# Kernel tuning notes

Measured on AMD Instinct MI355X. Metric: run time of the kernel, lower is better.

## Reference

```python
import jax, jax.numpy as jnp
import numpy as np
from jax import lax

EPS = 1e-5  # torch LayerNorm / BatchNorm1d default eps
HEADS, DH, DEPTH, C = 4, 128, 2, 512


def setup_inputs() -> dict:
    key = jax.random.key(0)
    ks = iter(jax.random.split(key, 48))
    def rn(shape, scale=1.0):
        return jax.random.normal(next(ks), shape, jnp.float32) * scale
    d, L = 1024, DEPTH
    inp = {}
    inp['x'] = rn((16, 10, 256, d))                      # (b, ncrops, T, d)
    # Temporal embedding: Conv1d(d -> 512, k=3, pad=1) + ReLU
    inp['W_emb'] = rn((C, d, 3), (d * 3) ** -0.5)
    inp['b_emb'] = jnp.zeros((C,), jnp.float32)
    # Transformer (depth=2), params stacked along layer axis
    inp['ln1_g'] = jnp.ones((L, C), jnp.float32); inp['ln1_b'] = jnp.zeros((L, C), jnp.float32)
    inp['W_qkv'] = rn((L, C, 4 * HEADS * DH), C ** -0.5)  # to_qkv (no bias), inner_dim*4 = 2048
    inp['W_o']  = rn((L, 2 * HEADS * DH, C), (2 * HEADS * DH) ** -0.5)
    inp['b_o']  = jnp.zeros((L, C), jnp.float32)
    inp['ln2_g'] = jnp.ones((L, C), jnp.float32); inp['ln2_b'] = jnp.zeros((L, C), jnp.float32)
    inp['W_f1'] = rn((L, C, C), C ** -0.5); inp['b_f1'] = jnp.zeros((L, C), jnp.float32)
    inp['W_f2'] = rn((L, C, C), C ** -0.5); inp['b_f2'] = jnp.zeros((L, C), jnp.float32)
    # NormalHead: conv1 512->32 (k=1), bn1, conv2 32->16 (k=1), bn2, conv3 16->1 (k=1)
    inp['c1_W'] = rn((32, C), C ** -0.5); inp['c1_b'] = jnp.zeros((32,), jnp.float32)
    inp['bn1_g'] = jnp.ones((32,), jnp.float32); inp['bn1_b'] = jnp.zeros((32,), jnp.float32)
    inp['bn1_m'] = rn((32,), 0.1)
    inp['bn1_v'] = jax.random.uniform(next(ks), (32,), jnp.float32, 0.5, 1.5)
    inp['c2_W'] = rn((16, 32), 32 ** -0.5); inp['c2_b'] = jnp.zeros((16,), jnp.float32)
    inp['bn2_g'] = jnp.ones((16,), jnp.float32); inp['bn2_b'] = jnp.zeros((16,), jnp.float32)
    inp['bn2_m'] = rn((16,), 0.1)
    inp['bn2_v'] = jax.random.uniform(next(ks), (16,), jnp.float32, 0.5, 1.5)
    inp['c3_W'] = rn((1, 16), 0.25); inp['c3_b'] = jnp.zeros((1,), jnp.float32)
    return inp


def _ln(z, g, b):
    m = z.mean(-1, keepdims=True)
    v = ((z - m) ** 2).mean(-1, keepdims=True)
    return (z - m) / jnp.sqrt(v + EPS) * g + b


def _bn_eval(z, g, b, m, v):  # z: (B, C, T), eval-mode BatchNorm1d
    return (z - m[None, :, None]) / jnp.sqrt(v[None, :, None] + EPS) * g[None, :, None] + b[None, :, None]


def _k1conv(z, W, b):  # pointwise Conv1d: z (B, Ci, T), W (Co, Ci)
    return jnp.einsum('bct,oc->bot', z, W) + b[None, :, None]


def reference(x, W_emb, b_emb, ln1_g, ln1_b, W_qkv, W_o, b_o, ln2_g, ln2_b,
              W_f1, b_f1, W_f2, b_f2, c1_W, c1_b, bn1_g, bn1_b, bn1_m, bn1_v,
              c2_W, c2_b, bn2_g, bn2_b, bn2_m, bn2_v, c3_W, c3_b):
    b, n, T, d = x.shape
    h = x.reshape(b * n, T, d)
    # Temporal embedding: Conv1d(k=3, pad=1) + ReLU
    h = lax.conv_general_dilated(h.transpose(0, 2, 1), W_emb, (1,), 'SAME',
                                 dimension_numbers=('NCH', 'OIH', 'NCH'))
    h = jax.nn.relu(h + b_emb[None, :, None]).transpose(0, 2, 1)  # (BN, T, 512)

    # fixed positional-decay attention map attn2 (T, T), batch-independent
    idx = jnp.arange(T, dtype=jnp.float32)
    tg = jnp.abs(idx[None, :] - idx[:, None])
    a2 = jnp.exp(-tg / jnp.exp(1.0))
    a2 = a2 / a2.sum(-1)  # NOTE: broadcast over last axis, exactly as in the torch code

    scale = DH ** -0.5
    for l in range(DEPTH):
        z = _ln(h, ln1_g[l], ln1_b[l])
        qkvt = z @ W_qkv[l]                                   # (BN, T, 2048)
        q, k, v, t = jnp.split(qkvt, 4, axis=-1)
        def to_heads(u):
            return u.reshape(u.shape[0], T, HEADS, DH).transpose(0, 2, 1, 3)
        q, k, v, t = map(to_heads, (q, k, v, t))              # (BN, H, T, DH)
        attn1 = jax.nn.softmax(jnp.einsum('bhid,bhjd->bhij', q, k) * scale, axis=-1)
        o1 = jnp.einsum('bhij,bhjd->bhid', attn1, v)
        o2 = jnp.einsum('ij,bhjd->bhid', a2, t)
        o = jnp.concatenate([o1, o2], axis=-1)                # (BN, H, T, 2*DH)
        o = o.transpose(0, 2, 1, 3).reshape(h.shape[0], T, HEADS * 2 * DH)
        h = o @ W_o[l] + b_o[l] + h                           # attn residual
        z = _ln(h, ln2_g[l], ln2_b[l])
        h = (jax.nn.gelu(z @ W_f1[l] + b_f1[l], approximate=False) @ W_f2[l] + b_f2[l]) + h

    # NormalHead on (BN, C, T)
    f = h.transpose(0, 2, 1)
    x1 = _k1conv(f, c1_W, c1_b)                               # (BN, 32, T)
    x2 = _k1conv(jax.nn.relu(_bn_eval(x1, bn1_g, bn1_b, bn1_m, bn1_v)), c2_W, c2_b)  # (BN, 16, T)
    scores = jax.nn.sigmoid(_k1conv(jax.nn.relu(_bn_eval(x2, bn2_g, bn2_b, bn2_m, bn2_v)), c3_W, c3_b))
    normal_scores = scores.reshape(b, n, T).mean(1)           # mean over ncrops -> (b, T)

    def maha(feats, anchor, var):  # Mahalanobis distance vs BN running stats (no eps, as in source)
        dist = jnp.sqrt(jnp.sum((feats - anchor[None, :, None]) ** 2 / var[None, :, None], axis=1))
        return dist.reshape(b, n, T).mean(1)

    distance_sum = maha(x1, bn1_m, bn1_v) + maha(x2, bn2_m, bn2_v)
    return distance_sum * normal_scores                       # (b, T)
```

## Files before the change

kernel.cpp:

```cpp
#include <hip/hip_runtime.h>
#include <math.h>

#define T_    256
#define D_    1024
#define C_    512
#define H_    4
#define DH_   128
#define BNB   160
#define LEPS  1e-5f
#define INV_E 0.36787944117144233f
#define SCALE_ 0.08838834764831845f
#define LDT   40
#define XROW  264192

typedef unsigned short ushort;
typedef unsigned int   uint;
typedef __attribute__((ext_vector_type(8))) short short8;
typedef __attribute__((ext_vector_type(4))) float f32x4;

__device__ __forceinline__ ushort f2b(float f) {
    uint u = __float_as_uint(f);
    u += 0x7fffu + ((u >> 16) & 1u);
    return (ushort)(u >> 16);
}
__device__ __forceinline__ float b2f(ushort u) {
    return __uint_as_float(((uint)u) << 16);
}
__device__ __forceinline__ uint pk(float a, float b) {
    return (uint)f2b(a) | ((uint)f2b(b) << 16);
}
__device__ __forceinline__ void gl2lds(const void* g, void* l) {
    __builtin_amdgcn_global_load_lds(
        (const __attribute__((address_space(1))) void*)g,
        (__attribute__((address_space(3))) void*)l, 16, 0, 0);
}

__global__ void zero_k(float* __restrict__ p, int n) {
    int i = blockIdx.x * 256 + threadIdx.x;
    if (i < n) p[i] = 0.0f;
}

__global__ void xcvt_k(const float* __restrict__ src, ushort* __restrict__ dst, int n4) {
    int i = blockIdx.x * 256 + threadIdx.x;
    if (i < n4) {
        float4 f = ((const float4*)src)[i];
        uint2 v;
        v.x = pk(f.x, f.y);
        v.y = pk(f.z, f.w);
        int e   = i * 4;
        int bn  = e >> 18;
        int rem = e & 262143;
        ((uint2*)(dst + (size_t)bn * XROW + 1024 + rem))[0] = v;
    }
}

__global__ void xpad_k(ushort* __restrict__ dst, int nbn) {
    int i = blockIdx.x * 256 + threadIdx.x;
    if (i >= nbn * 1024) return;
    int bn = i >> 10, j = i & 1023;
    int r = j >> 9, c = j & 511;
    uint* base = (uint*)(dst + (size_t)bn * XROW);
    base[(r ? (XROW - 1024) / 2 : 0) + c] = 0u;
}

__global__ __launch_bounds__(256)
void tconv_k(const float* __restrict__ src, ushort* __restrict__ dst,
             int K, int N) {
    __shared__ float tile[32][33];
    int kb = blockIdx.x * 32, nb = blockIdx.y * 32;
    int tx = threadIdx.x & 31, ty = threadIdx.x >> 5;
#pragma unroll
    for (int i = 0; i < 32; i += 8)
        tile[ty + i][tx] = src[(size_t)(kb + ty + i) * N + nb + tx];
    __syncthreads();
#pragma unroll
    for (int i = 0; i < 32; i += 8)
        dst[(size_t)(nb + ty + i) * K + kb + tx] = f2b(tile[tx][ty + i]);
}

__global__ void bcvt_k(const float* __restrict__ src, ushort* __restrict__ dst, int n) {
    int i = blockIdx.x * 256 + threadIdx.x;
    if (i < n) dst[i] = f2b(src[i]);
}

__global__ void wemb_k(const float* __restrict__ W, ushort* __restrict__ Wt) {
    int idx = blockIdx.x * 256 + threadIdx.x;
    if (idx >= C_ * 3072) return;
    int c = idx / 3072, k = idx % 3072;
    int dt = k >> 10, ci = k & 1023;
    Wt[idx] = f2b(W[(size_t)c * 3072 + ci * 3 + dt]);
}

__global__ void a2_colsum_k(float* __restrict__ s) {
    int j = threadIdx.x;
    float acc = 0.0f;
    for (int k = 0; k < T_; k++) acc += expf(-fabsf((float)(j - k)) * INV_E);
    s[j] = acc;
}

__global__ void a2fill_k(const float* __restrict__ s, ushort* __restrict__ A2) {
    int i = blockIdx.x, j = threadIdx.x;
    A2[i * 256 + j] = f2b(expf(-fabsf((float)(i - j)) * INV_E) / s[j]);
}

__global__ __launch_bounds__(256)
void ln_k(const ushort* __restrict__ X, const float* __restrict__ g,
          const float* __restrict__ b, ushort* __restrict__ Z) {
    int row  = blockIdx.x * 4 + (threadIdx.x >> 6);
    int lane = threadIdx.x & 63;
    const ushort* xr = X + (size_t)row * C_ + lane * 8;
    uint4 raw = *(const uint4*)xr;
    float f[8];
    f[0] = __uint_as_float(raw.x << 16); f[1] = __uint_as_float(raw.x & 0xffff0000u);
    f[2] = __uint_as_float(raw.y << 16); f[3] = __uint_as_float(raw.y & 0xffff0000u);
    f[4] = __uint_as_float(raw.z << 16); f[5] = __uint_as_float(raw.z & 0xffff0000u);
    f[6] = __uint_as_float(raw.w << 16); f[7] = __uint_as_float(raw.w & 0xffff0000u);
    float s = 0.0f, s2 = 0.0f;
#pragma unroll
    for (int u = 0; u < 8; u++) { s += f[u]; s2 += f[u] * f[u]; }
#pragma unroll
    for (int m = 1; m < 64; m <<= 1) {
        s  += __shfl_xor(s, m);
        s2 += __shfl_xor(s2, m);
    }
    float mean = s * (1.0f / C_);
    float var  = s2 * (1.0f / C_) - mean * mean;
    float rinv = rsqrtf(var + LEPS);
    const float* gp = g + lane * 8;
    const float* bp = b + lane * 8;
    float4 g0 = *(const float4*)gp, g1 = *(const float4*)(gp + 4);
    float4 b0 = *(const float4*)bp, b1 = *(const float4*)(bp + 4);
    uint4 outv;
    outv.x = pk((f[0]-mean)*rinv*g0.x+b0.x, (f[1]-mean)*rinv*g0.y+b0.y);
    outv.y = pk((f[2]-mean)*rinv*g0.z+b0.z, (f[3]-mean)*rinv*g0.w+b0.w);
    outv.z = pk((f[4]-mean)*rinv*g1.x+b1.x, (f[5]-mean)*rinv*g1.y+b1.y);
    outv.w = pk((f[6]-mean)*rinv*g1.z+b1.z, (f[7]-mean)*rinv*g1.w+b1.w);
    *(uint4*)(Z + (size_t)row * C_ + lane * 8) = outv;
}

template<int CONV, int ACT, int RESID, int OUTBF>
__global__ __launch_bounds__(256)
void gemm_k(const ushort* __restrict__ A, const ushort* __restrict__ B,
            const float* __restrict__ bias, const ushort* __restrict__ R,
            void* __restrict__ Cout, int M, int N, int K,
            const ushort* __restrict__ Xp) {
    __shared__ __align__(16) ushort As[128 * 32];
    __shared__ __align__(16) ushort Bs[128 * 32];
    const int tid  = threadIdx.x;
    const int lane = tid & 63, wave = tid >> 6;
    const int wr = wave >> 1, wc = wave & 1;
    const int lm = lane & 15, quad = lane >> 4;

    const int NP = gridDim.x, My = gridDim.y;
    int m_idx, n_idx;
    if ((My & 7) == 0) {
        int bid = blockIdx.y * NP + blockIdx.x;
        m_idx = (bid & 7) + 8 * (bid / (8 * NP));
        n_idx = (bid >> 3) % NP;
    } else {
        m_idx = blockIdx.y; n_idx = blockIdx.x;
    }
    const int m0 = m_idx * 128, n0 = n_idx * 128;

    const int srow   = lane >> 2;
    const int schunk = (lane & 3) * 8;
    ushort* AsW = As + wave * 32 * 32;
    ushort* BsW = Bs + wave * 32 * 32;

    f32x4 acc[4][4];
#pragma unroll
    for (int mt = 0; mt < 4; mt++)
#pragma unroll
        for (int nt = 0; nt < 4; nt++) acc[mt][nt] = (f32x4){0.f, 0.f, 0.f, 0.f};

    for (int k0 = 0; k0 < K; k0 += 32) {
        if (CONV) {
            int dt = k0 >> 10;
            int ci = (k0 & 1023) + schunk;
            int g0 = m0 + wave * 32 + srow;
            int bn0 = g0 >> 8, t0 = g0 & 255;
            int g1 = g0 + 16;
            int bn1 = g1 >> 8, t1 = g1 & 255;
            gl2lds(Xp + (size_t)bn0 * XROW + (t0 + dt) * 1024 + ci, AsW);
            gl2lds(Xp + (size_t)bn1 * XROW + (t1 + dt) * 1024 + ci, AsW + 16 * 32);
        } else {
            const ushort* ga = A + (size_t)(m0 + wave * 32 + srow) * K + k0 + schunk;
            gl2lds(ga, AsW);
            gl2lds(ga + (size_t)16 * K, AsW + 16 * 32);
        }
        {
            const ushort* gb = B + (size_t)(n0 + wave * 32 + srow) * K + k0 + schunk;
            gl2lds(gb, BsW);
            gl2lds(gb + (size_t)16 * K, BsW + 16 * 32);
        }
        __syncthreads();
        short8 af[4], bfv[4];
#pragma unroll
        for (int mt = 0; mt < 4; mt++)
            af[mt] = *(const short8*)&As[(wr * 64 + mt * 16 + lm) * 32 + quad * 8];
#pragma unroll
        for (int nt = 0; nt < 4; nt++)
            bfv[nt] = *(const short8*)&Bs[(wc * 64 + nt * 16 + lm) * 32 + quad * 8];
#pragma unroll
        for (int mt = 0; mt < 4; mt++)
#pragma unroll
            for (int nt = 0; nt < 4; nt++)
                acc[mt][nt] = __builtin_amdgcn_mfma_f32_16x16x32_bf16(
                    af[mt], bfv[nt], acc[mt][nt], 0, 0, 0);
        __syncthreads();
    }

#pragma unroll
    for (int mt = 0; mt < 4; mt++) {
        int grow0 = m0 + wr * 64 + mt * 16 + quad * 4;
#pragma unroll
        for (int nt = 0; nt < 4; nt++) {
            int gcol = n0 + wc * 64 + nt * 16 + lm;
            float bia = bias ? bias[gcol] : 0.0f;
            f32x4 v = acc[mt][nt];
#pragma unroll
            for (int i = 0; i < 4; i++) {
                int grow = grow0 + i;
                float val = v[i] + bia;
                if (ACT == 1) val = val * 0.5f * (1.0f + erff(val * 0.70710678118654752f));
                if (ACT == 2) val = fmaxf(val, 0.0f);
                if (RESID) val += b2f(R[(size_t)grow * N + gcol]);
                if (OUTBF) ((ushort*)Cout)[(size_t)grow * N + gcol] = f2b(val);
                else       ((float*)Cout)[(size_t)grow * N + gcol]  = val;
            }
        }
    }
}

__global__ __launch_bounds__(256)
void attn1_k(const ushort* __restrict__ qkvt, ushort* __restrict__ O) {
    const int bn = blockIdx.x, h = blockIdx.y;
    const int tid = threadIdx.x;
    const int wave = tid >> 6, lane = tid & 63;
    const int lm = lane & 15, quad = lane >> 4;
    __shared__ __align__(16) ushort Ks[32 * 136];
    __shared__ __align__(16) ushort Vt[128 * 40];
    __shared__ __align__(16) ushort Ps[4][64 * 40];
    const ushort* base = qkvt + (size_t)bn * T_ * 2048;

    short8 aq[4][4];
#pragma unroll
    for (int mt = 0; mt < 4; mt++) {
        const ushort* qrow = base + (size_t)(wave * 64 + mt * 16 + lm) * 2048 + h * DH_;
#pragma unroll
        for (int ks = 0; ks < 4; ks++)
            aq[mt][ks] = *(const short8*)(qrow + ks * 32 + quad * 8);
    }

    f32x4 oacc[4][8];
#pragma unroll
    for (int mt = 0; mt < 4; mt++)
#pragma unroll
        for (int nt = 0; nt < 8; nt++) oacc[mt][nt] = (f32x4){0.f, 0.f, 0.f, 0.f};
    float mrow[4][4], lrow[4][4];
#pragma unroll
    for (int mt = 0; mt < 4; mt++)
#pragma unroll
        for (int i = 0; i < 4; i++) { mrow[mt][i] = -1e30f; lrow[mt][i] = 0.0f; }

    for (int kt = 0; kt < 8; kt++) {
        __syncthreads();
#pragma unroll
        for (int u = 0; u < 2; u++) {
            int ii = tid + u * 256;
            int j = ii >> 4, dc = ii & 15;
            *(uint4*)&Ks[j * 136 + dc * 8] =
                *(const uint4*)(base + (size_t)(kt * 32 + j) * 2048 + 512 + h * DH_ + dc * 8);
        }
        {
            int j = tid & 31, half = tid >> 5;
            const ushort* vrow = base + (size_t)(kt * 32 + j) * 2048 + 1024 + h * DH_ + half * 16;
            uint4 v0 = *(const uint4*)vrow;
            uint4 v1 = *(const uint4*)(vrow + 8);
            ushort e[16];
            *(uint4*)&e[0] = v0; *(uint4*)&e[8] = v1;
#pragma unroll
            for (int u = 0; u < 16; u++)
                Vt[(half * 16 + u) * 40 + j] = e[u];
        }
        __syncthreads();

        f32x4 s[4][2];
#pragma unroll
        for (int mt = 0; mt < 4; mt++)
#pragma unroll
            for (int nt = 0; nt < 2; nt++) s[mt][nt] = (f32x4){0.f, 0.f, 0.f, 0.f};
#pragma unroll
        for (int ks = 0; ks < 4; ks++) {
            short8 bk0 = *(const short8*)&Ks[lm * 136 + ks * 32 + quad * 8];
            short8 bk1 = *(const short8*)&Ks[(16 + lm) * 136 + ks * 32 + quad * 8];
#pragma unroll
            for (int mt = 0; mt < 4; mt++) {
                s[mt][0] = __builtin_amdgcn_mfma_f32_16x16x32_bf16(aq[mt][ks], bk0, s[mt][0], 0, 0, 0);
                s[mt][1] = __builtin_amdgcn_mfma_f32_16x16x32_bf16(aq[mt][ks], bk1, s[mt][1], 0, 0, 0);
            }
        }

#pragma unroll
        for (int mt = 0; mt < 4; mt++) {
#pragma unroll
            for (int i = 0; i < 4; i++) {
                float v0 = s[mt][0][i] * SCALE_;
                float v1 = s[mt][1][i] * SCALE_;
                float rmax = fmaxf(v0, v1);
#pragma unroll
                for (int mk = 1; mk < 16; mk <<= 1)
                    rmax = fmaxf(rmax, __shfl_xor(rmax, mk));
                float mold = mrow[mt][i];
                float mnew = fmaxf(mold, rmax);
                float alpha = __expf(mold - mnew);
                float p0 = __expf(v0 - mnew);
                float p1 = __expf(v1 - mnew);
                float rs = p0 + p1;
#pragma unroll
                for (int mk = 1; mk < 16; mk <<= 1)
                    rs += __shfl_xor(rs, mk);
                lrow[mt][i] = lrow[mt][i] * alpha + rs;
                mrow[mt][i] = mnew;
#pragma unroll
                for (int nt = 0; nt < 8; nt++) {
                    oacc[mt][nt][i] *= alpha;
                }
                int prow = mt * 16 + quad * 4 + i;
                Ps[wave][prow * 40 + lm]      = f2b(p0);
                Ps[wave][prow * 40 + 16 + lm] = f2b(p1);
            }
        }

        short8 ap[4];
#pragma unroll
        for (int mt = 0; mt < 4; mt++)
            ap[mt] = *(const short8*)&Ps[wave][(mt * 16 + lm) * 40 + quad * 8];
#pragma unroll
        for (int nt = 0; nt < 8; nt++) {
            short8 bv = *(const short8*)&Vt[(nt * 16 + lm) * 40 + quad * 8];
#pragma unroll
            for (int mt = 0; mt < 4; mt++)
                oacc[mt][nt] = __builtin_amdgcn_mfma_f32_16x16x32_bf16(ap[mt], bv, oacc[mt][nt], 0, 0, 0);
        }
    }

#pragma unroll
    for (int mt = 0; mt < 4; mt++) {
#pragma unroll
        for (int i = 0; i < 4; i++) {
            int row = wave * 64 + mt * 16 + quad * 4 + i;
            float rinv = 1.0f / lrow[mt][i];
#pragma unroll
            for (int nt = 0; nt < 8; nt++) {
                int d = nt * 16 + lm;
                O[((size_t)bn * T_ + row) * 1024 + h * 256 + d] =
                    f2b(oacc[mt][nt][i] * rinv);
            }
        }
    }
}

__global__ __launch_bounds__(256)
void attn2_k(const ushort* __restrict__ A2, const ushort* __restrict__ qkvt,
             ushort* __restrict__ O) {
    __shared__ __align__(16) ushort As[128 * LDT];
    __shared__ __align__(16) ushort Bs[128 * 48];
    const int tid = threadIdx.x;
    const int bn = blockIdx.z;
    const int m0 = blockIdx.y * 128;
    const int n0 = blockIdx.x * 128;
    const int lane = tid & 63, wave = tid >> 6;
    const int wr = wave >> 1, wc = wave & 1;
    const int lm = lane & 15, quad = lane >> 4;
    const ushort* tbase = qkvt + (size_t)bn * T_ * 2048 + 1536;
    const int r = tid >> 1, c0 = (tid & 1) * 2;

    f32x4 acc[4][4];
#pragma unroll
    for (int mt = 0; mt < 4; mt++)
#pragma unroll
        for (int nt = 0; nt < 4; nt++) acc[mt][nt] = (f32x4){0.f, 0.f, 0.f, 0.f};

    for (int k0 = 0; k0 < 256; k0 += 32) {
        const ushort* Arow = A2 + (size_t)(m0 + r) * 256 + k0;
        *(uint4*)&As[r * LDT + c0 * 8]       = *(const uint4*)(Arow + c0 * 8);
        *(uint4*)&As[r * LDT + (c0 + 1) * 8] = *(const uint4*)(Arow + (c0 + 1) * 8);
        {
            int kr = tid & 31, np = tid >> 5;
            const ushort* trow = tbase + (size_t)(k0 + kr) * 2048 + n0 + np * 16;
            uint4 v0 = *(const uint4*)trow;
            uint4 v1 = *(const uint4*)(trow + 8);
            ushort e[16];
            *(uint4*)&e[0] = v0; *(uint4*)&e[8] = v1;
#pragma unroll
            for (int u = 0; u < 16; u++)
                Bs[(np * 16 + u) * 48 + kr] = e[u];
        }
        __syncthreads();
        short8 af[4], bf[4];
#pragma unroll
        for (int mt = 0; mt < 4; mt++)
            af[mt] = *(const short8*)&As[(wr * 64 + mt * 16 + lm) * LDT + quad * 8];
#pragma unroll
        for (int nt = 0; nt < 4; nt++)
            bf[nt] = *(const short8*)&Bs[(wc * 64 + nt * 16 + lm) * 48 + quad * 8];
#pragma unroll
        for (int mt = 0; mt < 4; mt++)
#pragma unroll
            for (int nt = 0; nt < 4; nt++)
                acc[mt][nt] = __builtin_amdgcn_mfma_f32_16x16x32_bf16(
                    af[mt], bf[nt], acc[mt][nt], 0, 0, 0);
        __syncthreads();
    }

#pragma unroll
    for (int mt = 0; mt < 4; mt++) {
        int row0 = m0 + wr * 64 + mt * 16 + quad * 4;
#pragma unroll
        for (int nt = 0; nt < 4; nt++) {
            int n = n0 + wc * 64 + nt * 16 + lm;
            int h = n >> 7, d = n & 127;
#pragma unroll
            for (int i = 0; i < 4; i++) {
                int row = row0 + i;
                O[((size_t)bn * T_ + row) * 1024 + h * 256 + 128 + d] =
                    f2b(acc[mt][nt][i]);
            }
        }
    }
}

#define BLD 520
__global__ __launch_bounds__(256)
void head1_k(const ushort* __restrict__ Hb, const ushort* __restrict__ c1Wb,
             const float* __restrict__ c1b, float* __restrict__ X1) {
    __shared__ __align__(16) ushort As[128 * LDT];
    __shared__ __align__(16) ushort Bs[32 * BLD];
    const int tid = threadIdx.x;
    const int lane = tid & 63, wave = tid >> 6;
    const int lm = lane & 15, quad = lane >> 4;
    const int m0 = blockIdx.x * 128;
#pragma unroll
    for (int u = 0; u < 8; u++) {
        int ii = tid + u * 256;
        int nrow = ii >> 6;
        int koff = (ii & 63) * 8;
        *(uint4*)&Bs[nrow * BLD + koff] = *(const uint4*)(c1Wb + nrow * 512 + koff);
    }
    f32x4 acc[2][2];
#pragma unroll
    for (int mt = 0; mt < 2; mt++)
#pragma unroll
        for (int nt = 0; nt < 2; nt++) acc[mt][nt] = (f32x4){0.f, 0.f, 0.f, 0.f};

    const int r = tid >> 1, half = tid & 1;
    for (int k0 = 0; k0 < 512; k0 += 32) {
        const ushort* s = Hb + (size_t)(m0 + r) * 512 + k0 + half * 16;
        uint4 v0 = *(const uint4*)s;
        uint4 v1 = *(const uint4*)(s + 8);
        __syncthreads();
        *(uint4*)&As[r * LDT + half * 16]     = v0;
        *(uint4*)&As[r * LDT + half * 16 + 8] = v1;
        __syncthreads();
        short8 af[2], bf[2];
#pragma unroll
        for (int mt = 0; mt < 2; mt++)
            af[mt] = *(const short8*)&As[(wave * 32 + mt * 16 + lm) * LDT + quad * 8];
#pragma unroll
        for (int nt = 0; nt < 2; nt++)
            bf[nt] = *(const short8*)&Bs[(nt * 16 + lm) * BLD + k0 + quad * 8];
#pragma unroll
        for (int mt = 0; mt < 2; mt++)
#pragma unroll
            for (int nt = 0; nt < 2; nt++)
                acc[mt][nt] = __builtin_amdgcn_mfma_f32_16x16x32_bf16(
                    af[mt], bf[nt], acc[mt][nt], 0, 0, 0);
    }
#pragma unroll
    for (int mt = 0; mt < 2; mt++) {
        int row0 = m0 + wave * 32 + mt * 16 + quad * 4;
#pragma unroll
        for (int nt = 0; nt < 2; nt++) {
            int col = nt * 16 + lm;
            float bia = c1b[col];
#pragma unroll
            for (int i = 0; i < 4; i++)
                X1[(size_t)(row0 + i) * 32 + col] = acc[mt][nt][i] + bia;
        }
    }
}

__global__ __launch_bounds__(256)
void head2_k(const float* __restrict__ X1, int bn_base, int M,
             const float* __restrict__ g1, const float* __restrict__ b1,
             const float* __restrict__ m1, const float* __restrict__ v1,
             const float* __restrict__ c2W, const float* __restrict__ c2b,
             const float* __restrict__ g2, const float* __restrict__ b2,
             const float* __restrict__ m2, const float* __restrict__ v2,
             const float* __restrict__ c3W, const float* __restrict__ c3b,
             float* __restrict__ sum_dist, float* __restrict__ sum_score) {
    int row = blockIdx.x * 256 + threadIdx.x;
    if (row >= M) return;
    float x1[32], y1[32];
    const float* xr = X1 + (size_t)row * 32;
#pragma unroll
    for (int c = 0; c < 32; c++) x1[c] = xr[c];
    float d1 = 0.0f;
#pragma unroll
    for (int c = 0; c < 32; c++) {
        float dd = x1[c] - m1[c];
        d1 += dd * dd / v1[c];
        y1[c] = fmaxf(0.0f, dd * rsqrtf(v1[c] + LEPS) * g1[c] + b1[c]);
    }
    float d2 = 0.0f, sc = c3b[0];
#pragma unroll
    for (int o = 0; o < 16; o++) {
        float acc = c2b[o];
        const float* wr = c2W + o * 32;
#pragma unroll
        for (int c = 0; c < 32; c++) acc += wr[c] * y1[c];
        float dd = acc - m2[o];
        d2 += dd * dd / v2[o];
        float y2 = fmaxf(0.0f, dd * rsqrtf(v2[o] + LEPS) * g2[o] + b2[o]);
        sc += c3W[o] * y2;
    }
    float dist = sqrtf(d1) + sqrtf(d2);
    sc = 1.0f / (1.0f + expf(-sc));
    int bn = bn_base + (row >> 8);
    int t = row & 255;
    int b = bn / 10;
    atomicAdd(&sum_dist[b * T_ + t], dist);
    atomicAdd(&sum_score[b * T_ + t], sc);
}

__global__ void combine_k(const float* __restrict__ sd, const float* __restrict__ ss,
                          float* __restrict__ out) {
    int i = blockIdx.x * 256 + threadIdx.x;
    if (i < 16 * T_) out[i] = (sd[i] * 0.1f) * (ss[i] * 0.1f);
}

extern "C" void kernel_launch(void* const* d_in, const int* in_sizes, int n_in,
                              void* d_out, int out_size, void* d_ws, size_t ws_size,
                              hipStream_t stream) {
    const float* x     = (const float*)d_in[0];
    const float* W_emb = (const float*)d_in[1];
    const float* b_emb = (const float*)d_in[2];
    const float* ln1_g = (const float*)d_in[3];
    const float* ln1_b = (const float*)d_in[4];
    const float* W_qkv = (const float*)d_in[5];
    const float* W_o   = (const float*)d_in[6];
    const float* b_o   = (const float*)d_in[7];
    const float* ln2_g = (const float*)d_in[8];
    const float* ln2_b = (const float*)d_in[9];
    const float* W_f1  = (const float*)d_in[10];
    const float* b_f1  = (const float*)d_in[11];
    const float* W_f2  = (const float*)d_in[12];
    const float* b_f2  = (const float*)d_in[13];
    const float* c1_W  = (const float*)d_in[14];
    const float* c1_b  = (const float*)d_in[15];
    const float* bn1_g = (const float*)d_in[16];
    const float* bn1_b = (const float*)d_in[17];
    const float* bn1_m = (const float*)d_in[18];
    const float* bn1_v = (const float*)d_in[19];
    const float* c2_W  = (const float*)d_in[20];
    const float* c2_b  = (const float*)d_in[21];
    const float* bn2_g = (const float*)d_in[22];
    const float* bn2_b = (const float*)d_in[23];
    const float* bn2_m = (const float*)d_in[24];
    const float* bn2_v = (const float*)d_in[25];
    const float* c3_W  = (const float*)d_in[26];
    const float* c3_b  = (const float*)d_in[27];
    float* out = (float*)d_out;

    char* p = (char*)d_ws;
    auto alloc = [&](size_t bytes) -> char* {
        char* q = p; p += (bytes + 255) & ~(size_t)255; return q;
    };
    ushort* wEmb = (ushort*)alloc((size_t)C_ * 3072 * 2);
    ushort* wQkv = (ushort*)alloc((size_t)2 * 2048 * 512 * 2);
    ushort* wO   = (ushort*)alloc((size_t)2 * 512 * 1024 * 2);
    ushort* wF1  = (ushort*)alloc((size_t)2 * 512 * 512 * 2);
    ushort* wF2  = (ushort*)alloc((size_t)2 * 512 * 512 * 2);
    ushort* A2bf = (ushort*)alloc((size_t)256 * 256 * 2);
    ushort* c1Wb = (ushort*)alloc((size_t)32 * 512 * 2);
    float*  s256      = (float*)alloc(256 * 4);
    float*  sum_dist  = (float*)alloc(4096 * 4);
    float*  sum_score = (float*)alloc(4096 * 4);
    size_t fixedB = (size_t)(p - (char*)d_ws);

    int CH = 8;
    const int cands[7] = {160, 80, 40, 32, 20, 16, 10};
    for (int ci = 0; ci < 7; ci++) {
        size_t per = (size_t)cands[ci] * 256 * 10384 + 16384;
        if (fixedB + per <= ws_size) { CH = cands[ci]; break; }
    }
    const int MR = CH * 256;
    ushort* xbp  = (ushort*)alloc((size_t)CH * XROW * 2);
    ushort* h    = (ushort*)alloc((size_t)MR * 512 * 2);
    ushort* z    = (ushort*)alloc((size_t)MR * 512 * 2);
    ushort* qkvt = (ushort*)alloc((size_t)MR * 2048 * 2);
    ushort* o    = (ushort*)alloc((size_t)MR * 1024 * 2);
    ushort* g    = o;
    float*  X1   = (float*)alloc((size_t)MR * 32 * 4);

    zero_k<<<(8192 + 255) / 256, 256, 0, stream>>>(sum_dist, 8192);
    a2_colsum_k<<<1, 256, 0, stream>>>(s256);
    a2fill_k<<<256, 256, 0, stream>>>(s256, A2bf);
    wemb_k<<<(C_ * 3072 + 255) / 256, 256, 0, stream>>>(W_emb, wEmb);
    bcvt_k<<<(32 * 512 + 255) / 256, 256, 0, stream>>>(c1_W, c1Wb, 32 * 512);
    for (int l = 0; l < 2; l++) {
        tconv_k<<<dim3(512 / 32, 2048 / 32), 256, 0, stream>>>(
            W_qkv + (size_t)l * 512 * 2048, wQkv + (size_t)l * 2048 * 512, 512, 2048);
        tconv_k<<<dim3(1024 / 32, 512 / 32), 256, 0, stream>>>(
            W_o + (size_t)l * 1024 * 512, wO + (size_t)l * 512 * 1024, 1024, 512);
        tconv_k<<<dim3(512 / 32, 512 / 32), 256, 0, stream>>>(
            W_f1 + (size_t)l * 512 * 512, wF1 + (size_t)l * 512 * 512, 512, 512);
        tconv_k<<<dim3(512 / 32, 512 / 32), 256, 0, stream>>>(
            W_f2 + (size_t)l * 512 * 512, wF2 + (size_t)l * 512 * 512, 512, 512);
    }

    for (int cs = 0; cs < BNB; cs += CH) {
        const float* xc = x + (size_t)cs * T_ * D_;

        int n4 = MR * 1024 / 4;
        xcvt_k<<<(n4 + 255) / 256, 256, 0, stream>>>(xc, xbp, n4);
        xpad_k<<<(CH * 1024 + 255) / 256, 256, 0, stream>>>(xbp, CH);

        gemm_k<1, 2, 0, 1><<<dim3(512 / 128, MR / 128), 256, 0, stream>>>(
            nullptr, wEmb, b_emb, nullptr, h, MR, 512, 3072, xbp);

        for (int l = 0; l < 2; l++) {
            ln_k<<<MR / 4, 256, 0, stream>>>(h, ln1_g + l * C_, ln1_b + l * C_, z);
            gemm_k<0, 0, 0, 1><<<dim3(2048 / 128, MR / 128), 256, 0, stream>>>(
                z, wQkv + (size_t)l * 2048 * 512, nullptr, nullptr, qkvt,
                MR, 2048, 512, nullptr);
            attn1_k<<<dim3(CH, H_), 256, 0, stream>>>(qkvt, o);
            attn2_k<<<dim3(4, 2, CH), 256, 0, stream>>>(A2bf, qkvt, o);
            gemm_k<0, 0, 1, 1><<<dim3(512 / 128, MR / 128), 256, 0, stream>>>(
                o, wO + (size_t)l * 512 * 1024, b_o + l * C_, h, h,
                MR, 512, 1024, nullptr);
            ln_k<<<MR / 4, 256, 0, stream>>>(h, ln2_g + l * C_, ln2_b + l * C_, z);
            gemm_k<0, 1, 0, 1><<<dim3(512 / 128, MR / 128), 256, 0, stream>>>(
                z, wF1 + (size_t)l * 512 * 512, b_f1 + l * C_, nullptr, g,
                MR, 512, 512, nullptr);
            gemm_k<0, 0, 1, 1><<<dim3(512 / 128, MR / 128), 256, 0, stream>>>(
                g, wF2 + (size_t)l * 512 * 512, b_f2 + l * C_, h, h,
                MR, 512, 512, nullptr);
        }

        head1_k<<<MR / 128, 256, 0, stream>>>(h, c1Wb, c1_b, X1);
        head2_k<<<MR / 256, 256, 0, stream>>>(
            X1, cs, MR, bn1_g, bn1_b, bn1_m, bn1_v,
            c2_W, c2_b, bn2_g, bn2_b, bn2_m, bn2_v, c3_W, c3_b,
            sum_dist, sum_score);
    }

    combine_k<<<16, 256, 0, stream>>>(sum_dist, sum_score, out);
}
```

Baseline: 1.580 ms.

## Replace 128x128 GEMM with 256x256 double-buffered, swizzled, pipelined MFMA kernel

Replaces the simple 128x128-tile GEMM, which synchronised twice per 32-wide K step, with a 256x256-tile, 512-thread kernel using 64-wide K tiles. Global-to-LDS staging is double-buffered and prefetched up to two tiles ahead, with explicit vmcnt waits, barriers and raised wave priority around the MFMA blocks. An XOR swizzle on the LDS layout is added to avoid bank conflicts. The larger tiles give more reuse but leave fewer blocks for the small N=512 GEMMs (2 column tiles), and the 128 KB of LDS per block may limit occupancy.

```diff
diff --git a/kernel.cpp b/kernel.cpp
--- a/kernel.cpp
+++ b/kernel.cpp
@@ -138,17 +138,86 @@
     *(uint4*)(Z + (size_t)row * C_ + lane * 8) = outv;
 }
 
+
+#define VMW_8 asm volatile("s_waitcnt vmcnt(8)" ::: "memory")
+#define VMW_4 asm volatile("s_waitcnt vmcnt(4)" ::: "memory")
+#define VMW_2 asm volatile("s_waitcnt vmcnt(2)" ::: "memory")
+#define VMW_0 asm volatile("s_waitcnt vmcnt(0)" ::: "memory")
+#define VMW_N
+#define BAR() __builtin_amdgcn_s_barrier()
+#define LGK0() do { asm volatile("s_waitcnt lgkmcnt(0)" ::: "memory"); \
+                    __builtin_amdgcn_sched_barrier(0); } while (0)
+
+#define TILE(kt, S1, S2, S3, S4, W1, W2, W4) do {                              \
+                               \
+    _Pragma("unroll") for (int mf = 0; mf < 4; mf++)                           \
+      _Pragma("unroll") for (int ks = 0; ks < 2; ks++)                         \
+        af[mf][ks] = ldA(kt, mf, ks);                                          \
+    _Pragma("unroll") for (int nf = 0; nf < 2; nf++)                           \
+      _Pragma("unroll") for (int ks = 0; ks < 2; ks++)                         \
+        bf[nf][ks] = ldB(kt, nf, ks);                                          \
+    if (S1) stageB((kt) + 1, 1);                                               \
+    VMW_##W1; BAR(); LGK0();                                                   \
+    __builtin_amdgcn_s_setprio(1);                                             \
+    _Pragma("unroll") for (int ks = 0; ks < 2; ks++)                           \
+      _Pragma("unroll") for (int mf = 0; mf < 4; mf++)                         \
+        _Pragma("unroll") for (int nf = 0; nf < 2; nf++)                       \
+          acc[mf][nf] = __builtin_amdgcn_mfma_f32_16x16x32_bf16(               \
+              af[mf][ks], bf[nf][ks], acc[mf][nf], 0, 0, 0);                   \
+    __builtin_amdgcn_s_setprio(0);                                             \
+    BAR();                                                                     \
+                \
+    _Pragma("unroll") for (int nf = 2; nf < 4; nf++)                           \
+      _Pragma("unroll") for (int ks = 0; ks < 2; ks++)                         \
+        bf[nf][ks] = ldB(kt, nf, ks);                                          \
+    if (S2) stageA((kt) + 1, 1);                                               \
+    VMW_##W2; BAR(); LGK0();                                                   \
+    __builtin_amdgcn_s_setprio(1);                                             \
+    _Pragma("unroll") for (int ks = 0; ks < 2; ks++)                           \
+      _Pragma("unroll") for (int mf = 0; mf < 4; mf++)                         \
+        _Pragma("unroll") for (int nf = 2; nf < 4; nf++)                       \
+          acc[mf][nf] = __builtin_amdgcn_mfma_f32_16x16x32_bf16(               \
+              af[mf][ks], bf[nf][ks], acc[mf][nf], 0, 0, 0);                   \
+    __builtin_amdgcn_s_setprio(0);                                             \
+    BAR();                                                                     \
+                               \
+    _Pragma("unroll") for (int mf = 0; mf < 4; mf++)                           \
+      _Pragma("unroll") for (int ks = 0; ks < 2; ks++)                         \
+        af[mf][ks] = ldA(kt, mf + 4, ks);                                      \
+    if (S3) stageA((kt) + 2, 0);                                               \
+    BAR(); LGK0();                                                             \
+    __builtin_amdgcn_s_setprio(1);                                             \
+    _Pragma("unroll") for (int ks = 0; ks < 2; ks++)                           \
+      _Pragma("unroll") for (int mf = 0; mf < 4; mf++)                         \
+        _Pragma("unroll") for (int nf = 0; nf < 2; nf++)                       \
+          acc[mf + 4][nf] = __builtin_amdgcn_mfma_f32_16x16x32_bf16(           \
+              af[mf][ks], bf[nf][ks], acc[mf + 4][nf], 0, 0, 0);               \
+    __builtin_amdgcn_s_setprio(0);                                             \
+    BAR();                                                                     \
+              \
+    if (S4) stageB((kt) + 2, 0);                                               \
+    VMW_##W4; BAR();                                                           \
+    __builtin_amdgcn_s_setprio(1);                                             \
+    _Pragma("unroll") for (int ks = 0; ks < 2; ks++)                           \
+      _Pragma("unroll") for (int mf = 0; mf < 4; mf++)                         \
+        _Pragma("unroll") for (int nf = 2; nf < 4; nf++)                       \
+          acc[mf + 4][nf] = __builtin_amdgcn_mfma_f32_16x16x32_bf16(           \
+              af[mf][ks], bf[nf][ks], acc[mf + 4][nf], 0, 0, 0);               \
+    __builtin_amdgcn_s_setprio(0);                                             \
+    BAR();                                                                     \
+} while (0)
+
 template<int CONV, int ACT, int RESID, int OUTBF>
-__global__ __launch_bounds__(256)
-void gemm_k(const ushort* __restrict__ A, const ushort* __restrict__ B,
-            const float* __restrict__ bias, const ushort* __restrict__ R,
-            void* __restrict__ Cout, int M, int N, int K,
-            const ushort* __restrict__ Xp) {
-    __shared__ __align__(16) ushort As[128 * 32];
-    __shared__ __align__(16) ushort Bs[128 * 32];
+__global__ __launch_bounds__(512, 2)
+void gemm256_k(const ushort* __restrict__ A, const ushort* __restrict__ B,
+               const float* __restrict__ bias, const ushort* __restrict__ R,
+               void* __restrict__ Cout, int M, int N, int K,
+               const ushort* __restrict__ Xp) {
+    __shared__ __align__(16) ushort As[32768];
+    __shared__ __align__(16) ushort Bs[32768];
     const int tid  = threadIdx.x;
-    const int lane = tid & 63, wave = tid >> 6;
-    const int wr = wave >> 1, wc = wave & 1;
+    const int wave = tid >> 6, lane = tid & 63;
+    const int wm = wave >> 2, wn = wave & 3;
     const int lm = lane & 15, quad = lane >> 4;
 
     const int NP = gridDim.x, My = gridDim.y;
@@ -160,64 +229,75 @@
     } else {
         m_idx = blockIdx.y; n_idx = blockIdx.x;
     }
-    const int m0 = m_idx * 128, n0 = n_idx * 128;
-
-    const int srow   = lane >> 2;
-    const int schunk = (lane & 3) * 8;
-    ushort* AsW = As + wave * 32 * 32;
-    ushort* BsW = Bs + wave * 32 * 32;
-
-    f32x4 acc[4][4];
-#pragma unroll
-    for (int mt = 0; mt < 4; mt++)
-#pragma unroll
-        for (int nt = 0; nt < 4; nt++) acc[mt][nt] = (f32x4){0.f, 0.f, 0.f, 0.f};
-
-    for (int k0 = 0; k0 < K; k0 += 32) {
+    const int m0 = m_idx * 256, n0 = n_idx * 256;
+
+    const int srow = lane >> 3;
+    const int scol = ((lane & 7) ^ srow) << 3;
+
+    auto stageA = [&](int kt, int half) {
+        ushort* lds = As + (((kt & 1) * 2 + half) << 13) + (wave << 9);
+        int r0 = half * 128 + wave * 8 + srow;
         if (CONV) {
+            int k0 = kt << 6;
             int dt = k0 >> 10;
-            int ci = (k0 & 1023) + schunk;
-            int g0 = m0 + wave * 32 + srow;
-            int bn0 = g0 >> 8, t0 = g0 & 255;
-            int g1 = g0 + 16;
-            int bn1 = g1 >> 8, t1 = g1 & 255;
-            gl2lds(Xp + (size_t)bn0 * XROW + (t0 + dt) * 1024 + ci, AsW);
-            gl2lds(Xp + (size_t)bn1 * XROW + (t1 + dt) * 1024 + ci, AsW + 16 * 32);
+            int cb = (k0 & 1023) + scol;
+            int g0 = m0 + r0;
+            gl2lds(Xp + (size_t)(g0 >> 8) * XROW + ((g0 & 255) + dt) * 1024 + cb, lds);
+            int g1 = g0 + 64;
+            gl2lds(Xp + (size_t)(g1 >> 8) * XROW + ((g1 & 255) + dt) * 1024 + cb, lds + 4096);
         } else {
-            const ushort* ga = A + (size_t)(m0 + wave * 32 + srow) * K + k0 + schunk;
-            gl2lds(ga, AsW);
-            gl2lds(ga + (size_t)16 * K, AsW + 16 * 32);
-        }
-        {
-            const ushort* gb = B + (size_t)(n0 + wave * 32 + srow) * K + k0 + schunk;
-            gl2lds(gb, BsW);
-            gl2lds(gb + (size_t)16 * K, BsW + 16 * 32);
-        }
-        __syncthreads();
-        short8 af[4], bfv[4];
-#pragma unroll
-        for (int mt = 0; mt < 4; mt++)
-            af[mt] = *(const short8*)&As[(wr * 64 + mt * 16 + lm) * 32 + quad * 8];
-#pragma unroll
-        for (int nt = 0; nt < 4; nt++)
-            bfv[nt] = *(const short8*)&Bs[(wc * 64 + nt * 16 + lm) * 32 + quad * 8];
-#pragma unroll
-        for (int mt = 0; mt < 4; mt++)
-#pragma unroll
-            for (int nt = 0; nt < 4; nt++)
-                acc[mt][nt] = __builtin_amdgcn_mfma_f32_16x16x32_bf16(
-                    af[mt], bfv[nt], acc[mt][nt], 0, 0, 0);
-        __syncthreads();
-    }
-
-#pragma unroll
-    for (int mt = 0; mt < 4; mt++) {
-        int grow0 = m0 + wr * 64 + mt * 16 + quad * 4;
-#pragma unroll
-        for (int nt = 0; nt < 4; nt++) {
-            int gcol = n0 + wc * 64 + nt * 16 + lm;
+            const ushort* ga = A + (size_t)(m0 + r0) * K + (kt << 6) + scol;
+            gl2lds(ga, lds);
+            gl2lds(ga + (size_t)64 * K, lds + 4096);
+        }
+    };
+    auto stageB = [&](int kt, int half) {
+        ushort* lds = Bs + (((kt & 1) * 2 + half) << 13) + (wave << 9);
+        const ushort* gb = B + (size_t)(n0 + half * 128 + wave * 8 + srow) * K
+                             + (kt << 6) + scol;
+        gl2lds(gb, lds);
+        gl2lds(gb + (size_t)64 * K, lds + 4096);
+    };
+
+    auto ldA = [&](int kt, int mf, int ks) -> short8 {
+        int r = wm * 16 + mf * 32 + lm;
+        int slot = (quad + ks * 4) ^ (lm & 7);
+        return *(const short8*)&As[(((kt & 1) * 2 + (r >> 7)) << 13)
+                                   + (r & 127) * 64 + slot * 8];
+    };
+    auto ldB = [&](int kt, int nf, int ks) -> short8 {
+        int r = wn * 16 + nf * 64 + lm;
+        int slot = (quad + ks * 4) ^ (lm & 7);
+        return *(const short8*)&Bs[(((kt & 1) * 2 + (r >> 7)) << 13)
+                                   + (r & 127) * 64 + slot * 8];
+    };
+
+    short8 af[4][2], bf[4][2];
+    f32x4 acc[8][4];
+#pragma unroll
+    for (int mf = 0; mf < 8; mf++)
+#pragma unroll
+        for (int nf = 0; nf < 4; nf++) acc[mf][nf] = (f32x4){0.f, 0.f, 0.f, 0.f};
+
+    const int NT = K >> 6;
+    stageA(0, 0); stageB(0, 0); stageB(0, 1); stageA(0, 1);
+    stageA(1, 0); stageB(1, 0);
+    VMW_8;
+    BAR();
+
+    for (int kt = 0; kt < NT - 2; kt++)
+        TILE(kt, 1, 1, 1, 1, 8, 8, 8);
+    TILE(NT - 2, 1, 1, 0, 0, 8, 8, 4);
+    TILE(NT - 1, 0, 0, 0, 0, 2, 0, N);
+
+#pragma unroll
+    for (int mf = 0; mf < 8; mf++) {
+        int grow0 = m0 + wm * 16 + mf * 32 + quad * 4;
+#pragma unroll
+        for (int nf = 0; nf < 4; nf++) {
+            int gcol = n0 + wn * 16 + nf * 64 + lm;
             float bia = bias ? bias[gcol] : 0.0f;
-            f32x4 v = acc[mt][nt];
+            f32x4 v = acc[mf][nf];
 #pragma unroll
             for (int i = 0; i < 4; i++) {
                 int grow = grow0 + i;
@@ -627,24 +707,24 @@
         xcvt_k<<<(n4 + 255) / 256, 256, 0, stream>>>(xc, xbp, n4);
         xpad_k<<<(CH * 1024 + 255) / 256, 256, 0, stream>>>(xbp, CH);
 
-        gemm_k<1, 2, 0, 1><<<dim3(512 / 128, MR / 128), 256, 0, stream>>>(
+        gemm256_k<1, 2, 0, 1><<<dim3(512 / 256, MR / 256), 512, 0, stream>>>(
             nullptr, wEmb, b_emb, nullptr, h, MR, 512, 3072, xbp);
 
         for (int l = 0; l < 2; l++) {
             ln_k<<<MR / 4, 256, 0, stream>>>(h, ln1_g + l * C_, ln1_b + l * C_, z);
-            gemm_k<0, 0, 0, 1><<<dim3(2048 / 128, MR / 128), 256, 0, stream>>>(
+            gemm256_k<0, 0, 0, 1><<<dim3(2048 / 256, MR / 256), 512, 0, stream>>>(
                 z, wQkv + (size_t)l * 2048 * 512, nullptr, nullptr, qkvt,
                 MR, 2048, 512, nullptr);
             attn1_k<<<dim3(CH, H_), 256, 0, stream>>>(qkvt, o);
             attn2_k<<<dim3(4, 2, CH), 256, 0, stream>>>(A2bf, qkvt, o);
-            gemm_k<0, 0, 1, 1><<<dim3(512 / 128, MR / 128), 256, 0, stream>>>(
+            gemm256_k<0, 0, 1, 1><<<dim3(512 / 256, MR / 256), 512, 0, stream>>>(
                 o, wO + (size_t)l * 512 * 1024, b_o + l * C_, h, h,
                 MR, 512, 1024, nullptr);
             ln_k<<<MR / 4, 256, 0, stream>>>(h, ln2_g + l * C_, ln2_b + l * C_, z);
-            gemm_k<0, 1, 0, 1><<<dim3(512 / 128, MR / 128), 256, 0, stream>>>(
+            gemm256_k<0, 1, 0, 1><<<dim3(512 / 256, MR / 256), 512, 0, stream>>>(
                 z, wF1 + (size_t)l * 512 * 512, b_f1 + l * C_, nullptr, g,
                 MR, 512, 512, nullptr);
-            gemm_k<0, 0, 1, 1><<<dim3(512 / 128, MR / 128), 256, 0, stream>>>(
+            gemm256_k<0, 0, 1, 1><<<dim3(512 / 256, MR / 256), 512, 0, stream>>>(
                 g, wF2 + (size_t)l * 512 * 512, b_f2 + l * C_, h, h,
                 MR, 512, 512, nullptr);
         }
```

New measurement: 1.677 ms. +6.2%, slower.
